# Performance work log

Measured on AMD Instinct MI355X. Metric: run time of the kernel, lower is better.

The kernel has to match this reference:

```python
import jax, jax.numpy as jnp
import numpy as np

P = 16; H_IMG = 384; W_IMG = 384; D = 1024
N_LAYERS = 24; DI = 2048; DS = 16; DTR = 64; DC = 4; EPS = 1e-5


def setup_inputs() -> dict:
    key = jax.random.key(0)
    ks = jax.random.split(key, 12)
    B = 2
    inp = {}
    inp["x"] = jax.random.normal(ks[0], (B, 3, H_IMG, W_IMG), jnp.float32)
    inp["patch_w"] = jax.random.normal(ks[1], (D, 3, P, P), jnp.float32) * 0.02
    inp["patch_b"] = jnp.zeros((D,), jnp.float32)
    inp["pos_embed"] = jax.random.normal(ks[2], (1, (H_IMG // P) * (W_IMG // P), D), jnp.float32) * 0.02
    inp["ln_g"] = jnp.ones((N_LAYERS, D), jnp.float32)
    inp["ln_b"] = jnp.zeros((N_LAYERS, D), jnp.float32)
    inp["in_w"] = jax.random.normal(ks[3], (N_LAYERS, 2 * DI, D), jnp.float32) * 0.02
    inp["conv_w"] = jax.random.normal(ks[4], (N_LAYERS, DI, DC), jnp.float32) * 0.1
    inp["conv_b"] = jnp.zeros((N_LAYERS, DI), jnp.float32)
    inp["xproj_w"] = jax.random.normal(ks[5], (N_LAYERS, DTR + 2 * DS, DI), jnp.float32) * 0.02
    inp["dt_w"] = jax.random.normal(ks[6], (N_LAYERS, DI, DTR), jnp.float32) * 0.02
    inp["dt_b"] = jnp.full((N_LAYERS, DI), -4.0, jnp.float32)  # softplus(-4) ~ 0.018
    inp["A_log"] = jnp.broadcast_to(jnp.log(jnp.arange(1, DS + 1, dtype=jnp.float32)), (N_LAYERS, DI, DS)).copy()
    inp["D_param"] = jnp.ones((N_LAYERS, DI), jnp.float32)
    inp["out_w"] = jax.random.normal(ks[7], (N_LAYERS, D, DI), jnp.float32) * 0.02
    return inp


def _layer_norm(x, g, b):
    mu = jnp.mean(x, axis=-1, keepdims=True)
    var = jnp.var(x, axis=-1, keepdims=True)
    return (x - mu) * jax.lax.rsqrt(var + EPS) * g + b


def _mamba_block(x, p):
    g, bn, Win, Wc, bc, Wxp, Wdt, bdt, Alog, Dd, Wout = p
    u = _layer_norm(x, g, bn)                          # [B,L,D]
    xz = jnp.einsum('bld,ed->ble', u, Win)             # [B,L,2*DI]
    xi, z = jnp.split(xz, 2, axis=-1)
    # causal depthwise conv1d along L (kernel DC=4)
    xt = jnp.moveaxis(xi, 1, 2)                        # [B,DI,L]
    L = xt.shape[-1]
    xpad = jnp.pad(xt, ((0, 0), (0, 0), (DC - 1, 0)))
    xc = sum(Wc[:, k][None, :, None] * xpad[:, :, k:k + L] for k in range(DC)) + bc[None, :, None]
    xc = jax.nn.silu(jnp.moveaxis(xc, 1, 2))           # [B,L,DI]
    dbc = jnp.einsum('bld,ed->ble', xc, Wxp)           # [B,L,DTR+2*DS]
    dt, Bm, Cm = jnp.split(dbc, [DTR, DTR + DS], axis=-1)
    dt = jax.nn.softplus(jnp.einsum('blr,dr->bld', dt, Wdt) + bdt)  # [B,L,DI]
    A = -jnp.exp(Alog)                                 # [DI,DS]
    dA = jnp.exp(dt[..., None] * A)                    # [B,L,DI,DS]
    dBx = (dt * xc)[..., None] * Bm[:, :, None, :]     # [B,L,DI,DS]

    def step(h, inp):
        dA_t, dBx_t, C_t = inp
        h = dA_t * h + dBx_t                           # [B,DI,DS]
        y = jnp.einsum('bds,bs->bd', h, C_t)
        return h, y

    h0 = jnp.zeros((x.shape[0], DI, DS), x.dtype)
    xs = (jnp.moveaxis(dA, 1, 0), jnp.moveaxis(dBx, 1, 0), jnp.moveaxis(Cm, 1, 0))
    _, ys = jax.lax.scan(step, h0, xs)                 # ys: [L,B,DI]
    y = jnp.moveaxis(ys, 0, 1) + Dd * xc
    y = y * jax.nn.silu(z)
    return x + jnp.einsum('ble,de->bld', y, Wout)


def _forward(x, patch_w, patch_b, pos_embed, ln_g, ln_b, in_w, conv_w, conv_b,
             xproj_w, dt_w, dt_b, A_log, D_param, out_w):
    feat = jax.lax.conv_general_dilated(
        x, patch_w, (P, P), 'VALID',
        dimension_numbers=('NCHW', 'OIHW', 'NCHW')) + patch_b[None, :, None, None]
    Bn, Dd, Hh, Ww = feat.shape
    tok = feat.reshape(Bn, Dd, Hh * Ww).transpose(0, 2, 1)  # [B,L,D]
    h0, w0 = H_IMG // P, W_IMG // P
    pe = pos_embed.reshape(1, h0, w0, Dd)
    pe = jax.image.resize(pe, (1, Hh, Ww, Dd), 'bilinear')  # align_corners=False
    tok = tok + pe.reshape(1, Hh * Ww, Dd)
    params = (ln_g, ln_b, in_w, conv_w, conv_b, xproj_w, dt_w, dt_b, A_log, D_param, out_w)

    def layer(carry, p):
        return jax.checkpoint(_mamba_block)(carry, p), None

    tok, _ = jax.lax.scan(layer, tok, params)
    return tok


def reference(x, patch_w, patch_b, pos_embed, ln_g, ln_b, in_w, conv_w, conv_b,
              xproj_w, dt_w, dt_b, A_log, D_param, out_w):
    return _forward(x, patch_w, patch_b, pos_embed, ln_g, ln_b, in_w, conv_w, conv_b,
                    xproj_w, dt_w, dt_b, A_log, D_param, out_w)
```

## Files before the change

### kernel.cpp

```cpp
#include <hip/hip_runtime.h>
#include <hip/hip_bf16.h>
#include <math.h>

#define PATCH   16
#define HIMG    384
#define WIMG    384
#define DMODEL  1024
#define NLAYERS 24
#define DI      2048
#define DSTATE  16
#define DTR     64
#define DC      4
#define LN_EPS  1e-5f
#define BATCH   2
#define GRIDTOK 24
#define LTOK    (GRIDTOK*GRIDTOK)
#define NTOK    (BATCH*LTOK)
#define KPATCH  (3*PATCH*PATCH)
#define NCH     16
#define LC      (LTOK/NCH)
#define PSTRIDE ((size_t)NTOK * 2 * DI)

typedef __attribute__((ext_vector_type(8))) short short8;
typedef __attribute__((ext_vector_type(4))) float f32x4;

__device__ __forceinline__ float sigmoidf_(float v) { return 1.f / (1.f + __expf(-v)); }
__device__ __forceinline__ unsigned short f2bf(float f) {
    __hip_bfloat16 h = __float2bfloat16(f);
    return *(unsigned short*)&h;
}

__device__ __forceinline__ int xcd_swizzle(int orig, int nwg) {
    const int q = nwg >> 3, r = nwg & 7;
    const int xcd = orig & 7, idx = orig >> 3;
    return (xcd < r ? xcd * (q + 1) : r * (q + 1) + (xcd - r) * q) + idx;
}
__device__ __forceinline__ void swz_xyz(int& bx, int& by, int& bz) {
    const int gx = gridDim.x, gy = gridDim.y;
    const int nwg = gx * gy * gridDim.z;
    const int orig = blockIdx.x + gx * (blockIdx.y + gy * blockIdx.z);
    const int id = xcd_swizzle(orig, nwg);
    bx = id % gx;
    const int rest = id / gx;
    by = rest % gy;
    bz = rest / gy;
}

__global__ void f2bf_kernel(const float* __restrict__ in, unsigned short* __restrict__ out, int n4) {
    for (int i = blockIdx.x * blockDim.x + threadIdx.x; i < n4; i += gridDim.x * blockDim.x) {
        const float4 v = ((const float4*)in)[i];
        ushort4 o;
        o.x = f2bf(v.x); o.y = f2bf(v.y); o.z = f2bf(v.z); o.w = f2bf(v.w);
        ((ushort4*)out)[i] = o;
    }
}

__global__ void im2col_kernel(const float* __restrict__ x, unsigned short* __restrict__ xcol) {
    int idx = blockIdx.x * blockDim.x + threadIdx.x;
    if (idx >= NTOK * KPATCH) return;
    int t = idx / KPATCH, k = idx % KPATCH;
    int b = t / LTOK, hw = t % LTOK;
    int h = hw / GRIDTOK, w = hw % GRIDTOK;
    int c = k / (PATCH*PATCH), r = k % (PATCH*PATCH);
    int i = r / PATCH, j = r % PATCH;
    xcol[idx] = f2bf(x[(((size_t)(b*3 + c)*HIMG) + h*PATCH + i)*WIMG + w*PATCH + j]);
}

__global__ __launch_bounds__(256) void layernorm_kernel(
        const float* __restrict__ x, const float* __restrict__ g,
        const float* __restrict__ b, unsigned short* __restrict__ u) {
    const int t = blockIdx.x;
    const int tid = threadIdx.x;
    const float4 xv = ((const float4*)(x + (size_t)t * DMODEL))[tid];
    float s = xv.x + xv.y + xv.z + xv.w;
    float q = xv.x*xv.x + xv.y*xv.y + xv.z*xv.z + xv.w*xv.w;
    #pragma unroll
    for (int off = 32; off >= 1; off >>= 1) {
        s += __shfl_xor(s, off);
        q += __shfl_xor(q, off);
    }
    __shared__ float red[8];
    if ((tid & 63) == 0) { red[tid >> 6] = s; red[4 + (tid >> 6)] = q; }
    __syncthreads();
    s = red[0] + red[1] + red[2] + red[3];
    q = red[4] + red[5] + red[6] + red[7];
    const float mu   = s * (1.f / DMODEL);
    const float var  = q * (1.f / DMODEL) - mu * mu;
    const float rstd = rsqrtf(var + LN_EPS);
    const float4 gv = ((const float4*)g)[tid];
    const float4 bv = ((const float4*)b)[tid];
    ushort4 o;
    o.x = f2bf((xv.x - mu) * rstd * gv.x + bv.x);
    o.y = f2bf((xv.y - mu) * rstd * gv.y + bv.y);
    o.z = f2bf((xv.z - mu) * rstd * gv.z + bv.z);
    o.w = f2bf((xv.w - mu) * rstd * gv.w + bv.w);
    ((ushort4*)(u + (size_t)t * DMODEL))[tid] = o;
}

__global__ __launch_bounds__(256) void gemm_mfma_bt(
        const unsigned short* __restrict__ A, int lda,
        const float* __restrict__ B, int ldb,
        float* __restrict__ C, int M, int N, int Ksub) {
    __shared__ unsigned short As[128 * 64];
    __shared__ unsigned short Bs[128 * 64];
    int bx, by, bz;
    swz_xyz(bx, by, bz);
    const int tid = threadIdx.x;
    const int m0 = bx * 128;
    const int n0 = by * 128;
    const int koff = bz * Ksub;
    C += (size_t)bz * M * N;

    const int lane = tid & 63;
    const int wid  = tid >> 6;
    const int wm = (wid >> 1) * 64;
    const int wn = (wid & 1) * 64;
    const int fr = lane & 15;
    const int cb = lane >> 4;

    const int srow = tid >> 3;
    const int skc  = tid & 7;

    f32x4 acc[4][4];
    #pragma unroll
    for (int i = 0; i < 4; ++i)
        #pragma unroll
        for (int j = 0; j < 4; ++j) acc[i][j] = (f32x4){0.f, 0.f, 0.f, 0.f};

    uint4  areg[4];
    float4 breg[4][2];

    const int nk = Ksub / 64;
    #pragma unroll
    for (int i = 0; i < 4; ++i) {
        const int r = srow + 32 * i;
        areg[i] = *(const uint4*)(A + (size_t)(m0 + r) * lda + koff + skc * 8);
        const float* bp = B + (size_t)(n0 + r) * ldb + koff + skc * 8;
        breg[i][0] = *(const float4*)bp;
        breg[i][1] = *(const float4*)(bp + 4);
    }

    for (int ks = 0; ks < nk; ++ks) {
        __syncthreads();
        #pragma unroll
        for (int i = 0; i < 4; ++i) {
            const int r = srow + 32 * i;
            const int idx = r * 64 + ((skc ^ (r & 7)) << 3);
            *(uint4*)&As[idx] = areg[i];
            const float* bf = (const float*)&breg[i][0];
            short8 hv;
            #pragma unroll
            for (int j = 0; j < 8; ++j) hv[j] = (short)f2bf(bf[j]);
            *(short8*)&Bs[idx] = hv;
        }
        __syncthreads();
        if (ks + 1 < nk) {
            const int k1 = koff + (ks + 1) * 64;
            #pragma unroll
            for (int i = 0; i < 4; ++i) {
                const int r = srow + 32 * i;
                areg[i] = *(const uint4*)(A + (size_t)(m0 + r) * lda + k1 + skc * 8);
                const float* bp = B + (size_t)(n0 + r) * ldb + k1 + skc * 8;
                breg[i][0] = *(const float4*)bp;
                breg[i][1] = *(const float4*)(bp + 4);
            }
        }
        #pragma unroll
        for (int kk = 0; kk < 2; ++kk) {
            short8 af[4], bfr[4];
            #pragma unroll
            for (int mi = 0; mi < 4; ++mi) {
                const int row = wm + mi * 16 + fr;
                af[mi] = *(const short8*)&As[row * 64 + (((kk * 4 + cb) ^ (row & 7)) << 3)];
            }
            #pragma unroll
            for (int ni = 0; ni < 4; ++ni) {
                const int row = wn + ni * 16 + fr;
                bfr[ni] = *(const short8*)&Bs[row * 64 + (((kk * 4 + cb) ^ (row & 7)) << 3)];
            }
            #pragma unroll
            for (int mi = 0; mi < 4; ++mi)
                #pragma unroll
                for (int ni = 0; ni < 4; ++ni)
                    acc[mi][ni] = __builtin_amdgcn_mfma_f32_16x16x32_bf16(
                        af[mi], bfr[ni], acc[mi][ni], 0, 0, 0);
        }
    }

    #pragma unroll
    for (int mi = 0; mi < 4; ++mi) {
        const int rbase = m0 + wm + mi * 16 + cb * 4;
        #pragma unroll
        for (int ni = 0; ni < 4; ++ni) {
            const int col = n0 + wn + ni * 16 + fr;
            #pragma unroll
            for (int j = 0; j < 4; ++j)
                C[(size_t)(rbase + j) * N + col] = acc[mi][ni][j];
        }
    }
}

template<int EPI>
__global__ __launch_bounds__(256) void gemm_bb(
        const unsigned short* __restrict__ A, int lda,
        const unsigned short* __restrict__ B, int ldb,
        float* __restrict__ C, int M, int N, int Ksub,
        const float* __restrict__ bias, const float* __restrict__ aux) {
    __shared__ unsigned short As[128 * 64];
    __shared__ unsigned short Bs[128 * 64];
    int bx, by, bz;
    swz_xyz(bx, by, bz);
    const int tid = threadIdx.x;
    const int m0 = bx * 128;
    const int n0 = by * 128;

    const int lane = tid & 63;
    const int wid  = tid >> 6;
    const int wm = (wid >> 1) * 64;
    const int wn = (wid & 1) * 64;
    const int fr = lane & 15;
    const int cb = lane >> 4;
    const int srow = tid >> 3;
    const int skc  = tid & 7;

    f32x4 acc[4][4];
    #pragma unroll
    for (int i = 0; i < 4; ++i)
        #pragma unroll
        for (int j = 0; j < 4; ++j) acc[i][j] = (f32x4){0.f, 0.f, 0.f, 0.f};

    uint4 areg[4], breg[4];
    const int nk = Ksub / 64;
    #pragma unroll
    for (int i = 0; i < 4; ++i) {
        const int r = srow + 32 * i;
        areg[i] = *(const uint4*)(A + (size_t)(m0 + r) * lda + skc * 8);
        breg[i] = *(const uint4*)(B + (size_t)(n0 + r) * ldb + skc * 8);
    }

    for (int ks = 0; ks < nk; ++ks) {
        __syncthreads();
        #pragma unroll
        for (int i = 0; i < 4; ++i) {
            const int r = srow + 32 * i;
            const int idx = r * 64 + ((skc ^ (r & 7)) << 3);
            *(uint4*)&As[idx] = areg[i];
            *(uint4*)&Bs[idx] = breg[i];
        }
        __syncthreads();
        if (ks + 1 < nk) {
            const int k1 = (ks + 1) * 64;
            #pragma unroll
            for (int i = 0; i < 4; ++i) {
                const int r = srow + 32 * i;
                areg[i] = *(const uint4*)(A + (size_t)(m0 + r) * lda + k1 + skc * 8);
                breg[i] = *(const uint4*)(B + (size_t)(n0 + r) * ldb + k1 + skc * 8);
            }
        }
        #pragma unroll
        for (int kk = 0; kk < 2; ++kk) {
            short8 af[4], bfr[4];
            #pragma unroll
            for (int mi = 0; mi < 4; ++mi) {
                const int row = wm + mi * 16 + fr;
                af[mi] = *(const short8*)&As[row * 64 + (((kk * 4 + cb) ^ (row & 7)) << 3)];
            }
            #pragma unroll
            for (int ni = 0; ni < 4; ++ni) {
                const int row = wn + ni * 16 + fr;
                bfr[ni] = *(const short8*)&Bs[row * 64 + (((kk * 4 + cb) ^ (row & 7)) << 3)];
            }
            #pragma unroll
            for (int mi = 0; mi < 4; ++mi)
                #pragma unroll
                for (int ni = 0; ni < 4; ++ni)
                    acc[mi][ni] = __builtin_amdgcn_mfma_f32_16x16x32_bf16(
                        af[mi], bfr[ni], acc[mi][ni], 0, 0, 0);
        }
    }

    #pragma unroll
    for (int mi = 0; mi < 4; ++mi) {
        const int rbase = m0 + wm + mi * 16 + cb * 4;
        #pragma unroll
        for (int ni = 0; ni < 4; ++ni) {
            const int col = n0 + wn + ni * 16 + fr;
            #pragma unroll
            for (int j = 0; j < 4; ++j) {
                float v = acc[mi][ni][j];
                if (EPI == 1) {
                    v += bias[col];
                    v = (v > 20.f) ? v : log1pf(__expf(v));
                } else if (EPI == 2) {
                    v += bias[col] + aux[(size_t)((rbase + j) % LTOK) * DMODEL + col];
                }
                C[(size_t)(rbase + j) * N + col] = v;
            }
        }
    }
}

__global__ __launch_bounds__(256) void gemm_xproj(
        const unsigned short* __restrict__ A,
        const unsigned short* __restrict__ B,
        float* __restrict__ C) {
    __shared__ unsigned short As[128 * 64];
    __shared__ unsigned short Bs[96 * 64];
    int bx, by, bz;
    swz_xyz(bx, by, bz);
    const int tid = threadIdx.x;
    const int m0 = bx * 128;
    const int koff = by * (DI / 8);
    C += (size_t)by * NTOK * 96;

    const int lane = tid & 63;
    const int wid  = tid >> 6;
    const int wm = wid * 32;
    const int fr = lane & 15;
    const int cb = lane >> 4;
    const int srow = tid >> 3;
    const int skc  = tid & 7;

    f32x4 acc[2][6];
    #pragma unroll
    for (int i = 0; i < 2; ++i)
        #pragma unroll
        for (int j = 0; j < 6; ++j) acc[i][j] = (f32x4){0.f, 0.f, 0.f, 0.f};

    uint4 areg[4], breg[3];
    #pragma unroll
    for (int i = 0; i < 4; ++i)
        areg[i] = *(const uint4*)(A + (size_t)(m0 + srow + 32 * i) * DI + koff + skc * 8);
    #pragma unroll
    for (int i = 0; i < 3; ++i) {
        const int idx = tid + 256 * i;
        breg[i] = *(const uint4*)(B + (size_t)(idx >> 3) * DI + koff + (idx & 7) * 8);
    }

    const int nk = (DI / 8) / 64;
    for (int ks = 0; ks < nk; ++ks) {
        __syncthreads();
        #pragma unroll
        for (int i = 0; i < 4; ++i) {
            const int r = srow + 32 * i;
            *(uint4*)&As[r * 64 + ((skc ^ (r & 7)) << 3)] = areg[i];
        }
        #pragma unroll
        for (int i = 0; i < 3; ++i) {
            const int idx = tid + 256 * i;
            const int r = idx >> 3, kc = idx & 7;
            *(uint4*)&Bs[r * 64 + ((kc ^ (r & 7)) << 3)] = breg[i];
        }
        __syncthreads();
        if (ks + 1 < nk) {
            const int k1 = koff + (ks + 1) * 64;
            #pragma unroll
            for (int i = 0; i < 4; ++i)
                areg[i] = *(const uint4*)(A + (size_t)(m0 + srow + 32 * i) * DI + k1 + skc * 8);
            #pragma unroll
            for (int i = 0; i < 3; ++i) {
                const int idx = tid + 256 * i;
                breg[i] = *(const uint4*)(B + (size_t)(idx >> 3) * DI + k1 + (idx & 7) * 8);
            }
        }
        #pragma unroll
        for (int kk = 0; kk < 2; ++kk) {
            short8 af[2], bfr[6];
            #pragma unroll
            for (int mi = 0; mi < 2; ++mi) {
                const int row = wm + mi * 16 + fr;
                af[mi] = *(const short8*)&As[row * 64 + (((kk * 4 + cb) ^ (row & 7)) << 3)];
            }
            #pragma unroll
            for (int ni = 0; ni < 6; ++ni) {
                const int row = ni * 16 + fr;
                bfr[ni] = *(const short8*)&Bs[row * 64 + (((kk * 4 + cb) ^ (row & 7)) << 3)];
            }
            #pragma unroll
            for (int mi = 0; mi < 2; ++mi)
                #pragma unroll
                for (int ni = 0; ni < 6; ++ni)
                    acc[mi][ni] = __builtin_amdgcn_mfma_f32_16x16x32_bf16(
                        af[mi], bfr[ni], acc[mi][ni], 0, 0, 0);
        }
    }

    #pragma unroll
    for (int mi = 0; mi < 2; ++mi) {
        const int rbase = m0 + wm + mi * 16 + cb * 4;
        #pragma unroll
        for (int ni = 0; ni < 6; ++ni) {
            const int col = ni * 16 + fr;
            #pragma unroll
            for (int j = 0; j < 4; ++j)
                C[(size_t)(rbase + j) * 96 + col] = acc[mi][ni][j];
        }
    }
}

__global__ void reduce8_kernel(const float* __restrict__ part, float* __restrict__ out,
                               unsigned short* __restrict__ out64, int n) {
    int i = blockIdx.x * blockDim.x + threadIdx.x;
    if (i >= n) return;
    float s = 0.f;
    #pragma unroll
    for (int z = 0; z < 8; ++z) s += part[(size_t)z * n + i];
    out[i] = s;
    const int col = i % 96;
    if (col < 64) out64[(i / 96) * 64 + col] = f2bf(s);
}

__global__ void conv1d_silu_kernel(const float* __restrict__ xzP,
                                   const float* __restrict__ wc,
                                   const float* __restrict__ bc,
                                   float* __restrict__ xc,
                                   unsigned short* __restrict__ xc_bf) {
    int idx = blockIdx.x * blockDim.x + threadIdx.x;
    if (idx >= NTOK * DI) return;
    const int t = idx >> 11;
    const int e = idx & (DI - 1);
    const int l = t % LTOK;
    const float4 w = *(const float4*)(wc + e * DC);
    const float* xp0 = xzP + (size_t)t * (2*DI) + e;
    const float* xp1 = xp0 + PSTRIDE;
    float acc = bc[e] + w.w * (xp0[0] + xp1[0]);
    if (l >= 1) acc += w.z * (xp0[-(2*DI)]   + xp1[-(2*DI)]);
    if (l >= 2) acc += w.y * (xp0[-2*(2*DI)] + xp1[-2*(2*DI)]);
    if (l >= 3) acc += w.x * (xp0[-3*(2*DI)] + xp1[-3*(2*DI)]);
    const float r = acc * sigmoidf_(acc);
    xc[idx] = r;
    xc_bf[idx] = f2bf(r);
}

__global__ __launch_bounds__(256) void scan_pass1(
        const float* __restrict__ dt, const float* __restrict__ xc,
        const float* __restrict__ dbc, const float* __restrict__ Alog,
        float* __restrict__ Fst, float* __restrict__ sdt) {
    const int tid = threadIdx.x;
    const int e  = blockIdx.x * 256 + tid;
    const int c  = blockIdx.y;
    const int b  = blockIdx.z;
    const int l0 = c * LC;
    const size_t tb = (size_t)b * LTOK + l0;

    __shared__ float Bs[LC][16];
    for (int idx = tid; idx < LC * 16; idx += 256) {
        const int row = idx >> 4, s = idx & 15;
        Bs[row][s] = dbc[(tb + row) * 96 + 64 + s];
    }

    float Aval[DSTATE];
    {
        const float* ap = Alog + (size_t)e * DSTATE;
        #pragma unroll
        for (int s = 0; s < DSTATE; ++s) Aval[s] = -__expf(ap[s]);
    }
    __syncthreads();

    const float* dtp = dt + tb * DI + e;
    const float* xcp = xc + tb * DI + e;
    float h[DSTATE];
    #pragma unroll
    for (int s = 0; s < DSTATE; ++s) h[s] = 0.f;
    float sum_dt = 0.f;

    float dtv = dtp[0], xcv = xcp[0];
    for (int l = 0; l < LC; ++l) {
        float dtn = 0.f, xcn = 0.f;
        if (l + 1 < LC) { dtn = dtp[(size_t)(l+1) * DI]; xcn = xcp[(size_t)(l+1) * DI]; }
        sum_dt += dtv;
        const float dx = dtv * xcv;
        const float4* brow = (const float4*)&Bs[l][0];
        const float4 b0 = brow[0], b1 = brow[1], b2 = brow[2], b3 = brow[3];
        const float bb[16] = {b0.x,b0.y,b0.z,b0.w, b1.x,b1.y,b1.z,b1.w,
                              b2.x,b2.y,b2.z,b2.w, b3.x,b3.y,b3.z,b3.w};
        #pragma unroll
        for (int s = 0; s < DSTATE; ++s)
            h[s] = fmaf(__expf(dtv * Aval[s]), h[s], dx * bb[s]);
        dtv = dtn; xcv = xcn;
    }

    float4* Fp = (float4*)(Fst + ((((size_t)b * NCH + c) * DI) + e) * DSTATE);
    #pragma unroll
    for (int q = 0; q < 4; ++q)
        Fp[q] = make_float4(h[q*4+0], h[q*4+1], h[q*4+2], h[q*4+3]);
    sdt[((size_t)b * NCH + c) * DI + e] = sum_dt;
}

__global__ __launch_bounds__(256) void scan_pass3(
        const float* __restrict__ dt, const float* __restrict__ xc,
        const float* __restrict__ dbc, const float* __restrict__ xzP,
        const float* __restrict__ Alog, const float* __restrict__ Dp,
        const float* __restrict__ Fst, const float* __restrict__ sdt,
        unsigned short* __restrict__ y) {
    const int tid = threadIdx.x;
    const int e  = blockIdx.x * 256 + tid;
    const int c  = blockIdx.y;
    const int b  = blockIdx.z;
    const int l0 = c * LC;
    const size_t tb = (size_t)b * LTOK + l0;

    __shared__ float BCs[LC][32];
    for (int idx = tid; idx < LC * 32; idx += 256) {
        const int row = idx >> 5, col = idx & 31;
        BCs[row][col] = dbc[(tb + row) * 96 + 64 + col];
    }

    float Aval[DSTATE];
    {
        const float* ap = Alog + (size_t)e * DSTATE;
        #pragma unroll
        for (int s = 0; s < DSTATE; ++s) Aval[s] = -__expf(ap[s]);
    }
    const float Dv = Dp[e];

    float h[DSTATE];
    #pragma unroll
    for (int s = 0; s < DSTATE; ++s) h[s] = 0.f;
    for (int c2 = 0; c2 < c; ++c2) {
        const size_t base = ((size_t)b * NCH + c2) * DI + e;
        const float sd = sdt[base];
        const float4* Fp = (const float4*)(Fst + base * DSTATE);
        const float4 f0 = Fp[0], f1 = Fp[1], f2 = Fp[2], f3 = Fp[3];
        const float ff[16] = {f0.x,f0.y,f0.z,f0.w, f1.x,f1.y,f1.z,f1.w,
                              f2.x,f2.y,f2.z,f2.w, f3.x,f3.y,f3.z,f3.w};
        #pragma unroll
        for (int s = 0; s < DSTATE; ++s)
            h[s] = fmaf(__expf(Aval[s] * sd), h[s], ff[s]);
    }
    __syncthreads();

    const float* dtp = dt + tb * DI + e;
    const float* xcp = xc + tb * DI + e;
    const float* zp0 = xzP + tb * (2*DI) + DI + e;
    const float* zp1 = zp0 + PSTRIDE;
    unsigned short* yp = y + tb * DI + e;

    float dtv = dtp[0], xcv = xcp[0], zv = zp0[0] + zp1[0];
    for (int l = 0; l < LC; ++l) {
        float dtn = 0.f, xcn = 0.f, zn = 0.f;
        if (l + 1 < LC) {
            dtn = dtp[(size_t)(l+1) * DI];
            xcn = xcp[(size_t)(l+1) * DI];
            zn  = zp0[(size_t)(l+1) * (2*DI)] + zp1[(size_t)(l+1) * (2*DI)];
        }
        const float dx = dtv * xcv;
        const float4* brow = (const float4*)&BCs[l][0];
        const float4 b0 = brow[0], b1 = brow[1], b2 = brow[2], b3 = brow[3];
        const float4 c0 = brow[4], c1 = brow[5], c2 = brow[6], c3 = brow[7];
        const float bb[16] = {b0.x,b0.y,b0.z,b0.w, b1.x,b1.y,b1.z,b1.w,
                              b2.x,b2.y,b2.z,b2.w, b3.x,b3.y,b3.z,b3.w};
        const float cc[16] = {c0.x,c0.y,c0.z,c0.w, c1.x,c1.y,c1.z,c1.w,
                              c2.x,c2.y,c2.z,c2.w, c3.x,c3.y,c3.z,c3.w};
        float yv = 0.f;
        #pragma unroll
        for (int s = 0; s < DSTATE; ++s) {
            h[s] = fmaf(__expf(dtv * Aval[s]), h[s], dx * bb[s]);
            yv = fmaf(h[s], cc[s], yv);
        }
        yp[(size_t)l * DI] = f2bf((yv + Dv * xcv) * (zv * sigmoidf_(zv)));
        dtv = dtn; xcv = xcn; zv = zn;
    }
}

template<bool DO_LN>
__global__ __launch_bounds__(256) void reduce8_ln_kernel(
        const float* __restrict__ part, float* __restrict__ tok,
        const float* __restrict__ g, const float* __restrict__ b,
        unsigned short* __restrict__ u) {
    const int t = blockIdx.x;
    const int tid = threadIdx.x;
    const int n4 = NTOK * DMODEL / 4;
    const int i = t * 256 + tid;
    float4 tv = ((float4*)tok)[i];
    #pragma unroll
    for (int z = 0; z < 8; ++z) {
        const float4 p = ((const float4*)part)[(size_t)z * n4 + i];
        tv.x += p.x; tv.y += p.y; tv.z += p.z; tv.w += p.w;
    }
    ((float4*)tok)[i] = tv;
    if (DO_LN) {
        float s = tv.x + tv.y + tv.z + tv.w;
        float q = tv.x*tv.x + tv.y*tv.y + tv.z*tv.z + tv.w*tv.w;
        #pragma unroll
        for (int off = 32; off >= 1; off >>= 1) {
            s += __shfl_xor(s, off);
            q += __shfl_xor(q, off);
        }
        __shared__ float red[8];
        if ((tid & 63) == 0) { red[tid >> 6] = s; red[4 + (tid >> 6)] = q; }
        __syncthreads();
        s = red[0] + red[1] + red[2] + red[3];
        q = red[4] + red[5] + red[6] + red[7];
        const float mu   = s * (1.f / DMODEL);
        const float var  = q * (1.f / DMODEL) - mu * mu;
        const float rstd = rsqrtf(var + LN_EPS);
        const float4 gv = ((const float4*)g)[tid];
        const float4 bv = ((const float4*)b)[tid];
        ushort4 o;
        o.x = f2bf((tv.x - mu) * rstd * gv.x + bv.x);
        o.y = f2bf((tv.y - mu) * rstd * gv.y + bv.y);
        o.z = f2bf((tv.z - mu) * rstd * gv.z + bv.z);
        o.w = f2bf((tv.w - mu) * rstd * gv.w + bv.w);
        ((ushort4*)(u + (size_t)t * DMODEL))[tid] = o;
    }
}

extern "C" void kernel_launch(void* const* d_in, const int* in_sizes, int n_in,
                              void* d_out, int out_size, void* d_ws, size_t ws_size,
                              hipStream_t stream) {
    const float* x       = (const float*)d_in[0];
    const float* patch_w = (const float*)d_in[1];
    const float* patch_b = (const float*)d_in[2];
    const float* pos     = (const float*)d_in[3];
    const float* ln_g    = (const float*)d_in[4];
    const float* ln_b    = (const float*)d_in[5];
    const float* in_w    = (const float*)d_in[6];
    const float* conv_w  = (const float*)d_in[7];
    const float* conv_b  = (const float*)d_in[8];
    const float* xproj_w = (const float*)d_in[9];
    const float* dt_w    = (const float*)d_in[10];
    const float* dt_b    = (const float*)d_in[11];
    const float* A_log   = (const float*)d_in[12];
    const float* D_par   = (const float*)d_in[13];
    const float* out_w   = (const float*)d_in[14];

    float* tok = (float*)d_out;
    float* ws  = (float*)d_ws;
    float* xzP  = ws;  ws += 2 * PSTRIDE;
    float* xc   = ws;  ws += (size_t)NTOK * DI;
    float* dbcP = ws;  ws += (size_t)8 * NTOK * 96;
    float* dbc  = ws;  ws += (size_t)NTOK * 96;
    float* dtb  = ws;  ws += (size_t)NTOK * DI;
    float* Fst  = ws;  ws += (size_t)BATCH * NCH * DI * DSTATE;
    float* sdt  = ws;  ws += (size_t)BATCH * NCH * DI;
    unsigned short* us = (unsigned short*)ws;
    unsigned short* Xcol_bf  = us; us += (size_t)NTOK * KPATCH;
    unsigned short* u_bf     = us; us += (size_t)NTOK * DMODEL;
    unsigned short* xc_bf    = us; us += (size_t)NTOK * DI;
    unsigned short* yb_bf    = us; us += (size_t)NTOK * DI;
    unsigned short* dbc64_bf = us; us += (size_t)NTOK * 64;
    unsigned short* wxpb  = us; us += (size_t)NLAYERS * 96 * DI;
    unsigned short* wdtb  = us; us += (size_t)NLAYERS * DI * DTR;
    unsigned short* wpb   = us; us += (size_t)DMODEL * KPATCH;

    f2bf_kernel<<<1024, 256, 0, stream>>>(xproj_w, wxpb, NLAYERS*96*DI/4);
    f2bf_kernel<<<1024, 256, 0, stream>>>(dt_w,    wdtb, NLAYERS*DI*DTR/4);
    f2bf_kernel<<<256,  256, 0, stream>>>(patch_w, wpb,  DMODEL*KPATCH/4);

    im2col_kernel<<<(NTOK*KPATCH + 255)/256, 256, 0, stream>>>(x, Xcol_bf);
    gemm_bb<2><<<dim3(NTOK/128, DMODEL/128), 256, 0, stream>>>(
        Xcol_bf, KPATCH, wpb, KPATCH, tok, NTOK, DMODEL, KPATCH, patch_b, pos);

    layernorm_kernel<<<NTOK, 256, 0, stream>>>(tok, ln_g, ln_b, u_bf);

    for (int layer = 0; layer < NLAYERS; ++layer) {
        const float* Win = in_w  + (size_t)layer * 2 * DI * DMODEL;
        const float* Wo  = out_w + (size_t)layer * DMODEL * DI;
        const unsigned short* Wxp = wxpb + (size_t)layer * 96 * DI;
        const unsigned short* Wdt = wdtb + (size_t)layer * DI * DTR;
        const float* Wc  = conv_w + (size_t)layer * DI * DC;
        const float* Bc  = conv_b + (size_t)layer * DI;
        const float* Bdt = dt_b   + (size_t)layer * DI;
        const float* Al  = A_log  + (size_t)layer * DI * DSTATE;
        const float* Dd  = D_par  + (size_t)layer * DI;

        gemm_mfma_bt<<<dim3(NTOK/128, (2*DI)/128, 2), 256, 0, stream>>>(
            u_bf, DMODEL, Win, DMODEL, xzP, NTOK, 2*DI, DMODEL/2);
        conv1d_silu_kernel<<<(NTOK*DI + 255)/256, 256, 0, stream>>>(xzP, Wc, Bc, xc, xc_bf);
        gemm_xproj<<<dim3(NTOK/128, 8), 256, 0, stream>>>(xc_bf, Wxp, dbcP);
        reduce8_kernel<<<(NTOK*96 + 255)/256, 256, 0, stream>>>(dbcP, dbc, dbc64_bf, NTOK*96);
        gemm_bb<1><<<dim3(NTOK/128, DI/128), 256, 0, stream>>>(
            dbc64_bf, 64, Wdt, DTR, dtb, NTOK, DI, DTR, Bdt, nullptr);
        scan_pass1<<<dim3(DI/256, NCH, BATCH), 256, 0, stream>>>(
            dtb, xc, dbc, Al, Fst, sdt);
        scan_pass3<<<dim3(DI/256, NCH, BATCH), 256, 0, stream>>>(
            dtb, xc, dbc, xzP, Al, Dd, Fst, sdt, yb_bf);
        gemm_mfma_bt<<<dim3(NTOK/128, DMODEL/128, 8), 256, 0, stream>>>(
            yb_bf, DI, Wo, DI, xzP, NTOK, DMODEL, DI/8);
        if (layer < NLAYERS - 1)
            reduce8_ln_kernel<true><<<NTOK, 256, 0, stream>>>(
                xzP, tok, ln_g + (size_t)(layer+1) * DMODEL, ln_b + (size_t)(layer+1) * DMODEL, u_bf);
        else
            reduce8_ln_kernel<false><<<NTOK, 256, 0, stream>>>(
                xzP, tok, nullptr, nullptr, u_bf);
    }
}
```

Measured before the change: 4.495 ms.

## Retile fp32-weight GEMM to 128x64x128 tiles and cut split-K partials

Changes the bf16×fp32 GEMM tile from 128x128 with K-step 64 to 128x64 with K-step 128, with a new B-loading layout. The in-projection drops split-K entirely, which removes the summing of two partial buffers in the conv and scan kernels. The out-projection goes from 8-way to 4-way split-K, so the reduce+layernorm kernel reads half as many partials. The goal is less partial-sum traffic and fewer reduction reads. The cost is longer K loops per block and more A reloads, since each A tile is now shared across fewer N columns.

```diff
diff --git a/kernel.cpp b/kernel.cpp
--- a/kernel.cpp
+++ b/kernel.cpp
@@ -19,7 +19,6 @@
 #define KPATCH  (3*PATCH*PATCH)
 #define NCH     16
 #define LC      (LTOK/NCH)
-#define PSTRIDE ((size_t)NTOK * 2 * DI)
 
 typedef __attribute__((ext_vector_type(8))) short short8;
 typedef __attribute__((ext_vector_type(4))) float f32x4;
@@ -101,87 +100,99 @@
         const unsigned short* __restrict__ A, int lda,
         const float* __restrict__ B, int ldb,
         float* __restrict__ C, int M, int N, int Ksub) {
-    __shared__ unsigned short As[128 * 64];
-    __shared__ unsigned short Bs[128 * 64];
+    __shared__ unsigned short As[128 * 128];
+    __shared__ unsigned short Bs[64 * 128];
     int bx, by, bz;
     swz_xyz(bx, by, bz);
     const int tid = threadIdx.x;
     const int m0 = bx * 128;
-    const int n0 = by * 128;
+    const int n0 = by * 64;
     const int koff = bz * Ksub;
     C += (size_t)bz * M * N;
 
     const int lane = tid & 63;
     const int wid  = tid >> 6;
     const int wm = (wid >> 1) * 64;
-    const int wn = (wid & 1) * 64;
+    const int wn = (wid & 1) * 32;
     const int fr = lane & 15;
     const int cb = lane >> 4;
 
-    const int srow = tid >> 3;
-    const int skc  = tid & 7;
-
-    f32x4 acc[4][4];
+    const int srowA = tid >> 3;
+    const int skcA  = tid & 7;
+    const int browB = tid >> 2;
+    const int sb0   = (tid & 3) * 4;
+
+    f32x4 acc[4][2];
     #pragma unroll
     for (int i = 0; i < 4; ++i)
         #pragma unroll
-        for (int j = 0; j < 4; ++j) acc[i][j] = (f32x4){0.f, 0.f, 0.f, 0.f};
-
-    uint4  areg[4];
-    float4 breg[4][2];
-
-    const int nk = Ksub / 64;
+        for (int j = 0; j < 2; ++j) acc[i][j] = (f32x4){0.f, 0.f, 0.f, 0.f};
+
+    uint4  areg[4][2];
+    float4 bregf[8];
+
+    const int nk = Ksub / 128;
     #pragma unroll
     for (int i = 0; i < 4; ++i) {
-        const int r = srow + 32 * i;
-        areg[i] = *(const uint4*)(A + (size_t)(m0 + r) * lda + koff + skc * 8);
-        const float* bp = B + (size_t)(n0 + r) * ldb + koff + skc * 8;
-        breg[i][0] = *(const float4*)bp;
-        breg[i][1] = *(const float4*)(bp + 4);
+        const int r = srowA + 32 * i;
+        const unsigned short* ap = A + (size_t)(m0 + r) * lda + koff;
+        areg[i][0] = *(const uint4*)(ap + skcA * 8);
+        areg[i][1] = *(const uint4*)(ap + (skcA + 8) * 8);
+    }
+    {
+        const float* bp = B + (size_t)(n0 + browB) * ldb + koff + (tid & 3) * 32;
+        #pragma unroll
+        for (int j = 0; j < 8; ++j) bregf[j] = *(const float4*)(bp + j * 4);
     }
 
     for (int ks = 0; ks < nk; ++ks) {
         __syncthreads();
         #pragma unroll
         for (int i = 0; i < 4; ++i) {
-            const int r = srow + 32 * i;
-            const int idx = r * 64 + ((skc ^ (r & 7)) << 3);
-            *(uint4*)&As[idx] = areg[i];
-            const float* bf = (const float*)&breg[i][0];
+            const int r = srowA + 32 * i;
+            *(uint4*)&As[r * 128 + ((skcA       ^ (r & 7)) << 3)] = areg[i][0];
+            *(uint4*)&As[r * 128 + (((skcA + 8) ^ (r & 7)) << 3)] = areg[i][1];
+        }
+        #pragma unroll
+        for (int q = 0; q < 4; ++q) {
+            const float* f = (const float*)&bregf[2 * q];
             short8 hv;
             #pragma unroll
-            for (int j = 0; j < 8; ++j) hv[j] = (short)f2bf(bf[j]);
-            *(short8*)&Bs[idx] = hv;
+            for (int j = 0; j < 8; ++j) hv[j] = (short)f2bf(f[j]);
+            const int slot = sb0 + q;
+            *(short8*)&Bs[browB * 128 + ((slot ^ (browB & 7)) << 3)] = hv;
         }
         __syncthreads();
         if (ks + 1 < nk) {
-            const int k1 = koff + (ks + 1) * 64;
+            const int k1 = koff + (ks + 1) * 128;
             #pragma unroll
             for (int i = 0; i < 4; ++i) {
-                const int r = srow + 32 * i;
-                areg[i] = *(const uint4*)(A + (size_t)(m0 + r) * lda + k1 + skc * 8);
-                const float* bp = B + (size_t)(n0 + r) * ldb + k1 + skc * 8;
-                breg[i][0] = *(const float4*)bp;
-                breg[i][1] = *(const float4*)(bp + 4);
-            }
-        }
-        #pragma unroll
-        for (int kk = 0; kk < 2; ++kk) {
-            short8 af[4], bfr[4];
+                const int r = srowA + 32 * i;
+                const unsigned short* ap = A + (size_t)(m0 + r) * lda + k1;
+                areg[i][0] = *(const uint4*)(ap + skcA * 8);
+                areg[i][1] = *(const uint4*)(ap + (skcA + 8) * 8);
+            }
+            const float* bp = B + (size_t)(n0 + browB) * ldb + k1 + (tid & 3) * 32;
+            #pragma unroll
+            for (int j = 0; j < 8; ++j) bregf[j] = *(const float4*)(bp + j * 4);
+        }
+        #pragma unroll
+        for (int kk = 0; kk < 4; ++kk) {
+            short8 af[4], bfr[2];
             #pragma unroll
             for (int mi = 0; mi < 4; ++mi) {
                 const int row = wm + mi * 16 + fr;
-                af[mi] = *(const short8*)&As[row * 64 + (((kk * 4 + cb) ^ (row & 7)) << 3)];
-            }
-            #pragma unroll
-            for (int ni = 0; ni < 4; ++ni) {
+                af[mi] = *(const short8*)&As[row * 128 + (((kk * 4 + cb) ^ (row & 7)) << 3)];
+            }
+            #pragma unroll
+            for (int ni = 0; ni < 2; ++ni) {
                 const int row = wn + ni * 16 + fr;
-                bfr[ni] = *(const short8*)&Bs[row * 64 + (((kk * 4 + cb) ^ (row & 7)) << 3)];
+                bfr[ni] = *(const short8*)&Bs[row * 128 + (((kk * 4 + cb) ^ (row & 7)) << 3)];
             }
             #pragma unroll
             for (int mi = 0; mi < 4; ++mi)
                 #pragma unroll
-                for (int ni = 0; ni < 4; ++ni)
+                for (int ni = 0; ni < 2; ++ni)
                     acc[mi][ni] = __builtin_amdgcn_mfma_f32_16x16x32_bf16(
                         af[mi], bfr[ni], acc[mi][ni], 0, 0, 0);
         }
@@ -191,7 +202,7 @@
     for (int mi = 0; mi < 4; ++mi) {
         const int rbase = m0 + wm + mi * 16 + cb * 4;
         #pragma unroll
-        for (int ni = 0; ni < 4; ++ni) {
+        for (int ni = 0; ni < 2; ++ni) {
             const int col = n0 + wn + ni * 16 + fr;
             #pragma unroll
             for (int j = 0; j < 4; ++j)
@@ -410,7 +421,7 @@
     if (col < 64) out64[(i / 96) * 64 + col] = f2bf(s);
 }
 
-__global__ void conv1d_silu_kernel(const float* __restrict__ xzP,
+__global__ void conv1d_silu_kernel(const float* __restrict__ xz,
                                    const float* __restrict__ wc,
                                    const float* __restrict__ bc,
                                    float* __restrict__ xc,
@@ -421,12 +432,11 @@
     const int e = idx & (DI - 1);
     const int l = t % LTOK;
     const float4 w = *(const float4*)(wc + e * DC);
-    const float* xp0 = xzP + (size_t)t * (2*DI) + e;
-    const float* xp1 = xp0 + PSTRIDE;
-    float acc = bc[e] + w.w * (xp0[0] + xp1[0]);
-    if (l >= 1) acc += w.z * (xp0[-(2*DI)]   + xp1[-(2*DI)]);
-    if (l >= 2) acc += w.y * (xp0[-2*(2*DI)] + xp1[-2*(2*DI)]);
-    if (l >= 3) acc += w.x * (xp0[-3*(2*DI)] + xp1[-3*(2*DI)]);
+    const float* xp = xz + (size_t)t * (2*DI) + e;
+    float acc = bc[e] + w.w * xp[0];
+    if (l >= 1) acc += w.z * xp[-(2*DI)];
+    if (l >= 2) acc += w.y * xp[-2*(2*DI)];
+    if (l >= 3) acc += w.x * xp[-3*(2*DI)];
     const float r = acc * sigmoidf_(acc);
     xc[idx] = r;
     xc_bf[idx] = f2bf(r);
@@ -489,7 +499,7 @@
 
 __global__ __launch_bounds__(256) void scan_pass3(
         const float* __restrict__ dt, const float* __restrict__ xc,
-        const float* __restrict__ dbc, const float* __restrict__ xzP,
+        const float* __restrict__ dbc, const float* __restrict__ xz,
         const float* __restrict__ Alog, const float* __restrict__ Dp,
         const float* __restrict__ Fst, const float* __restrict__ sdt,
         unsigned short* __restrict__ y) {
@@ -532,17 +542,16 @@
 
     const float* dtp = dt + tb * DI + e;
     const float* xcp = xc + tb * DI + e;
-    const float* zp0 = xzP + tb * (2*DI) + DI + e;
-    const float* zp1 = zp0 + PSTRIDE;
+    const float* zp  = xz + tb * (2*DI) + DI + e;
     unsigned short* yp = y + tb * DI + e;
 
-    float dtv = dtp[0], xcv = xcp[0], zv = zp0[0] + zp1[0];
+    float dtv = dtp[0], xcv = xcp[0], zv = zp[0];
     for (int l = 0; l < LC; ++l) {
         float dtn = 0.f, xcn = 0.f, zn = 0.f;
         if (l + 1 < LC) {
             dtn = dtp[(size_t)(l+1) * DI];
             xcn = xcp[(size_t)(l+1) * DI];
-            zn  = zp0[(size_t)(l+1) * (2*DI)] + zp1[(size_t)(l+1) * (2*DI)];
+            zn  = zp[(size_t)(l+1) * (2*DI)];
         }
         const float dx = dtv * xcv;
         const float4* brow = (const float4*)&BCs[l][0];
@@ -564,7 +573,7 @@
 }
 
 template<bool DO_LN>
-__global__ __launch_bounds__(256) void reduce8_ln_kernel(
+__global__ __launch_bounds__(256) void reduce4_ln_kernel(
         const float* __restrict__ part, float* __restrict__ tok,
         const float* __restrict__ g, const float* __restrict__ b,
         unsigned short* __restrict__ u) {
@@ -574,7 +583,7 @@
     const int i = t * 256 + tid;
     float4 tv = ((float4*)tok)[i];
     #pragma unroll
-    for (int z = 0; z < 8; ++z) {
+    for (int z = 0; z < 4; ++z) {
         const float4 p = ((const float4*)part)[(size_t)z * n4 + i];
         tv.x += p.x; tv.y += p.y; tv.z += p.z; tv.w += p.w;
     }
@@ -627,7 +636,7 @@
 
     float* tok = (float*)d_out;
     float* ws  = (float*)d_ws;
-    float* xzP  = ws;  ws += 2 * PSTRIDE;
+    float* xz   = ws;  ws += (size_t)NTOK * 2 * DI;
     float* xc   = ws;  ws += (size_t)NTOK * DI;
     float* dbcP = ws;  ws += (size_t)8 * NTOK * 96;
     float* dbc  = ws;  ws += (size_t)NTOK * 96;
@@ -665,9 +674,9 @@
         const float* Al  = A_log  + (size_t)layer * DI * DSTATE;
         const float* Dd  = D_par  + (size_t)layer * DI;
 
-        gemm_mfma_bt<<<dim3(NTOK/128, (2*DI)/128, 2), 256, 0, stream>>>(
-            u_bf, DMODEL, Win, DMODEL, xzP, NTOK, 2*DI, DMODEL/2);
-        conv1d_silu_kernel<<<(NTOK*DI + 255)/256, 256, 0, stream>>>(xzP, Wc, Bc, xc, xc_bf);
+        gemm_mfma_bt<<<dim3(NTOK/128, (2*DI)/64, 1), 256, 0, stream>>>(
+            u_bf, DMODEL, Win, DMODEL, xz, NTOK, 2*DI, DMODEL);
+        conv1d_silu_kernel<<<(NTOK*DI + 255)/256, 256, 0, stream>>>(xz, Wc, Bc, xc, xc_bf);
         gemm_xproj<<<dim3(NTOK/128, 8), 256, 0, stream>>>(xc_bf, Wxp, dbcP);
         reduce8_kernel<<<(NTOK*96 + 255)/256, 256, 0, stream>>>(dbcP, dbc, dbc64_bf, NTOK*96);
         gemm_bb<1><<<dim3(NTOK/128, DI/128), 256, 0, stream>>>(
@@ -675,14 +684,14 @@
         scan_pass1<<<dim3(DI/256, NCH, BATCH), 256, 0, stream>>>(
             dtb, xc, dbc, Al, Fst, sdt);
         scan_pass3<<<dim3(DI/256, NCH, BATCH), 256, 0, stream>>>(
-            dtb, xc, dbc, xzP, Al, Dd, Fst, sdt, yb_bf);
-        gemm_mfma_bt<<<dim3(NTOK/128, DMODEL/128, 8), 256, 0, stream>>>(
-            yb_bf, DI, Wo, DI, xzP, NTOK, DMODEL, DI/8);
+            dtb, xc, dbc, xz, Al, Dd, Fst, sdt, yb_bf);
+        gemm_mfma_bt<<<dim3(NTOK/128, DMODEL/64, 4), 256, 0, stream>>>(
+            yb_bf, DI, Wo, DI, xz, NTOK, DMODEL, DI/4);
         if (layer < NLAYERS - 1)
-            reduce8_ln_kernel<true><<<NTOK, 256, 0, stream>>>(
-                xzP, tok, ln_g + (size_t)(layer+1) * DMODEL, ln_b + (size_t)(layer+1) * DMODEL, u_bf);
+            reduce4_ln_kernel<true><<<NTOK, 256, 0, stream>>>(
+                xz, tok, ln_g + (size_t)(layer+1) * DMODEL, ln_b + (size_t)(layer+1) * DMODEL, u_bf);
         else
-            reduce8_ln_kernel<false><<<NTOK, 256, 0, stream>>>(
-                xzP, tok, nullptr, nullptr, u_bf);
-    }
-}
+            reduce4_ln_kernel<false><<<NTOK, 256, 0, stream>>>(
+                xz, tok, nullptr, nullptr, u_bf);
+    }
+}
```

After: 5.807 ms. 29.2% more time.

## Retile x_proj split-K GEMM and add dedicated dt projection kernel

Applied to the files above, without the earlier changes.

The x_proj GEMM now uses 64-row tiles and a split-K factor of 16 instead of 128-row tiles with split 8. That launches four times as many workgroups, each doing a shorter K loop, and the reduction kernel now sums 16 partials. The dt projection (K=64) moves from the generic gemm_bb path to a specialized single-stage kernel with 128x64 tiles, which doubles its grid and drops the K loop. The intent is better CU occupancy for these small GEMMs, at the cost of more partial-sum traffic and a larger workspace.

```diff
diff --git a/kernel.cpp b/kernel.cpp
--- a/kernel.cpp
+++ b/kernel.cpp
@@ -20,6 +20,7 @@
 #define NCH     16
 #define LC      (LTOK/NCH)
 #define PSTRIDE ((size_t)NTOK * 2 * DI)
+#define XP_SK   16
 
 typedef __attribute__((ext_vector_type(8))) short short8;
 typedef __attribute__((ext_vector_type(4))) float f32x4;
@@ -288,62 +289,55 @@
             #pragma unroll
             for (int j = 0; j < 4; ++j) {
                 float v = acc[mi][ni][j];
-                if (EPI == 1) {
-                    v += bias[col];
-                    v = (v > 20.f) ? v : log1pf(__expf(v));
-                } else if (EPI == 2) {
+                if (EPI == 2)
                     v += bias[col] + aux[(size_t)((rbase + j) % LTOK) * DMODEL + col];
-                }
                 C[(size_t)(rbase + j) * N + col] = v;
             }
         }
     }
 }
 
-__global__ __launch_bounds__(256) void gemm_xproj(
+__global__ __launch_bounds__(256) void gemm_xproj64(
         const unsigned short* __restrict__ A,
         const unsigned short* __restrict__ B,
         float* __restrict__ C) {
-    __shared__ unsigned short As[128 * 64];
+    __shared__ unsigned short As[64 * 64];
     __shared__ unsigned short Bs[96 * 64];
     int bx, by, bz;
     swz_xyz(bx, by, bz);
     const int tid = threadIdx.x;
-    const int m0 = bx * 128;
-    const int koff = by * (DI / 8);
+    const int m0 = bx * 64;
+    const int koff = by * (DI / XP_SK);
     C += (size_t)by * NTOK * 96;
 
     const int lane = tid & 63;
     const int wid  = tid >> 6;
-    const int wm = wid * 32;
+    const int wm = wid * 16;
     const int fr = lane & 15;
     const int cb = lane >> 4;
     const int srow = tid >> 3;
     const int skc  = tid & 7;
 
-    f32x4 acc[2][6];
-    #pragma unroll
-    for (int i = 0; i < 2; ++i)
-        #pragma unroll
-        for (int j = 0; j < 6; ++j) acc[i][j] = (f32x4){0.f, 0.f, 0.f, 0.f};
-
-    uint4 areg[4], breg[3];
-    #pragma unroll
-    for (int i = 0; i < 4; ++i)
-        areg[i] = *(const uint4*)(A + (size_t)(m0 + srow + 32 * i) * DI + koff + skc * 8);
+    f32x4 acc[6];
+    #pragma unroll
+    for (int j = 0; j < 6; ++j) acc[j] = (f32x4){0.f, 0.f, 0.f, 0.f};
+
+    uint4 areg[2], breg[3];
+    areg[0] = *(const uint4*)(A + (size_t)(m0 + srow) * DI + koff + skc * 8);
+    areg[1] = *(const uint4*)(A + (size_t)(m0 + srow + 32) * DI + koff + skc * 8);
     #pragma unroll
     for (int i = 0; i < 3; ++i) {
         const int idx = tid + 256 * i;
         breg[i] = *(const uint4*)(B + (size_t)(idx >> 3) * DI + koff + (idx & 7) * 8);
     }
 
-    const int nk = (DI / 8) / 64;
+    const int nk = (DI / XP_SK) / 64;
     for (int ks = 0; ks < nk; ++ks) {
         __syncthreads();
-        #pragma unroll
-        for (int i = 0; i < 4; ++i) {
-            const int r = srow + 32 * i;
-            *(uint4*)&As[r * 64 + ((skc ^ (r & 7)) << 3)] = areg[i];
+        {
+            const int r0 = srow, r1 = srow + 32;
+            *(uint4*)&As[r0 * 64 + ((skc ^ (r0 & 7)) << 3)] = areg[0];
+            *(uint4*)&As[r1 * 64 + ((skc ^ (r1 & 7)) << 3)] = areg[1];
         }
         #pragma unroll
         for (int i = 0; i < 3; ++i) {
@@ -354,9 +348,8 @@
         __syncthreads();
         if (ks + 1 < nk) {
             const int k1 = koff + (ks + 1) * 64;
-            #pragma unroll
-            for (int i = 0; i < 4; ++i)
-                areg[i] = *(const uint4*)(A + (size_t)(m0 + srow + 32 * i) * DI + k1 + skc * 8);
+            areg[0] = *(const uint4*)(A + (size_t)(m0 + srow) * DI + k1 + skc * 8);
+            areg[1] = *(const uint4*)(A + (size_t)(m0 + srow + 32) * DI + k1 + skc * 8);
             #pragma unroll
             for (int i = 0; i < 3; ++i) {
                 const int idx = tid + 256 * i;
@@ -365,46 +358,115 @@
         }
         #pragma unroll
         for (int kk = 0; kk < 2; ++kk) {
-            short8 af[2], bfr[6];
-            #pragma unroll
-            for (int mi = 0; mi < 2; ++mi) {
-                const int row = wm + mi * 16 + fr;
-                af[mi] = *(const short8*)&As[row * 64 + (((kk * 4 + cb) ^ (row & 7)) << 3)];
-            }
+            const int arow = wm + fr;
+            const short8 af = *(const short8*)&As[arow * 64 + (((kk * 4 + cb) ^ (arow & 7)) << 3)];
+            short8 bfr[6];
             #pragma unroll
             for (int ni = 0; ni < 6; ++ni) {
                 const int row = ni * 16 + fr;
                 bfr[ni] = *(const short8*)&Bs[row * 64 + (((kk * 4 + cb) ^ (row & 7)) << 3)];
             }
             #pragma unroll
-            for (int mi = 0; mi < 2; ++mi)
-                #pragma unroll
-                for (int ni = 0; ni < 6; ++ni)
-                    acc[mi][ni] = __builtin_amdgcn_mfma_f32_16x16x32_bf16(
-                        af[mi], bfr[ni], acc[mi][ni], 0, 0, 0);
-        }
-    }
-
-    #pragma unroll
-    for (int mi = 0; mi < 2; ++mi) {
+            for (int ni = 0; ni < 6; ++ni)
+                acc[ni] = __builtin_amdgcn_mfma_f32_16x16x32_bf16(af, bfr[ni], acc[ni], 0, 0, 0);
+        }
+    }
+
+    const int rbase = m0 + wm + cb * 4;
+    #pragma unroll
+    for (int ni = 0; ni < 6; ++ni) {
+        const int col = ni * 16 + fr;
+        #pragma unroll
+        for (int j = 0; j < 4; ++j)
+            C[(size_t)(rbase + j) * 96 + col] = acc[ni][j];
+    }
+}
+
+__global__ __launch_bounds__(256) void gemm_dt(
+        const unsigned short* __restrict__ A,
+        const unsigned short* __restrict__ B,
+        float* __restrict__ C, const float* __restrict__ bias) {
+    __shared__ unsigned short As[128 * 64];
+    __shared__ unsigned short Bs[64 * 64];
+    int bx, by, bz;
+    swz_xyz(bx, by, bz);
+    const int tid = threadIdx.x;
+    const int m0 = bx * 128;
+    const int n0 = by * 64;
+
+    const int lane = tid & 63;
+    const int wid  = tid >> 6;
+    const int wm = (wid >> 1) * 64;
+    const int wn = (wid & 1) * 32;
+    const int fr = lane & 15;
+    const int cb = lane >> 4;
+    const int srow = tid >> 3;
+    const int skc  = tid & 7;
+
+    #pragma unroll
+    for (int i = 0; i < 4; ++i) {
+        const int r = srow + 32 * i;
+        const uint4 v = *(const uint4*)(A + (size_t)(m0 + r) * 64 + skc * 8);
+        *(uint4*)&As[r * 64 + ((skc ^ (r & 7)) << 3)] = v;
+    }
+    #pragma unroll
+    for (int i = 0; i < 2; ++i) {
+        const int r = srow + 32 * i;
+        const uint4 v = *(const uint4*)(B + (size_t)(n0 + r) * 64 + skc * 8);
+        *(uint4*)&Bs[r * 64 + ((skc ^ (r & 7)) << 3)] = v;
+    }
+    __syncthreads();
+
+    f32x4 acc[4][2];
+    #pragma unroll
+    for (int i = 0; i < 4; ++i)
+        #pragma unroll
+        for (int j = 0; j < 2; ++j) acc[i][j] = (f32x4){0.f, 0.f, 0.f, 0.f};
+
+    #pragma unroll
+    for (int kk = 0; kk < 2; ++kk) {
+        short8 af[4], bfr[2];
+        #pragma unroll
+        for (int mi = 0; mi < 4; ++mi) {
+            const int row = wm + mi * 16 + fr;
+            af[mi] = *(const short8*)&As[row * 64 + (((kk * 4 + cb) ^ (row & 7)) << 3)];
+        }
+        #pragma unroll
+        for (int ni = 0; ni < 2; ++ni) {
+            const int row = wn + ni * 16 + fr;
+            bfr[ni] = *(const short8*)&Bs[row * 64 + (((kk * 4 + cb) ^ (row & 7)) << 3)];
+        }
+        #pragma unroll
+        for (int mi = 0; mi < 4; ++mi)
+            #pragma unroll
+            for (int ni = 0; ni < 2; ++ni)
+                acc[mi][ni] = __builtin_amdgcn_mfma_f32_16x16x32_bf16(
+                    af[mi], bfr[ni], acc[mi][ni], 0, 0, 0);
+    }
+
+    #pragma unroll
+    for (int mi = 0; mi < 4; ++mi) {
         const int rbase = m0 + wm + mi * 16 + cb * 4;
         #pragma unroll
-        for (int ni = 0; ni < 6; ++ni) {
-            const int col = ni * 16 + fr;
-            #pragma unroll
-            for (int j = 0; j < 4; ++j)
-                C[(size_t)(rbase + j) * 96 + col] = acc[mi][ni][j];
-        }
-    }
-}
-
-__global__ void reduce8_kernel(const float* __restrict__ part, float* __restrict__ out,
-                               unsigned short* __restrict__ out64, int n) {
+        for (int ni = 0; ni < 2; ++ni) {
+            const int col = n0 + wn + ni * 16 + fr;
+            #pragma unroll
+            for (int j = 0; j < 4; ++j) {
+                float v = acc[mi][ni][j] + bias[col];
+                v = (v > 20.f) ? v : log1pf(__expf(v));
+                C[(size_t)(rbase + j) * DI + col] = v;
+            }
+        }
+    }
+}
+
+__global__ void reduce16_kernel(const float* __restrict__ part, float* __restrict__ out,
+                                unsigned short* __restrict__ out64, int n) {
     int i = blockIdx.x * blockDim.x + threadIdx.x;
     if (i >= n) return;
     float s = 0.f;
     #pragma unroll
-    for (int z = 0; z < 8; ++z) s += part[(size_t)z * n + i];
+    for (int z = 0; z < XP_SK; ++z) s += part[(size_t)z * n + i];
     out[i] = s;
     const int col = i % 96;
     if (col < 64) out64[(i / 96) * 64 + col] = f2bf(s);
@@ -629,7 +691,7 @@
     float* ws  = (float*)d_ws;
     float* xzP  = ws;  ws += 2 * PSTRIDE;
     float* xc   = ws;  ws += (size_t)NTOK * DI;
-    float* dbcP = ws;  ws += (size_t)8 * NTOK * 96;
+    float* dbcP = ws;  ws += (size_t)XP_SK * NTOK * 96;
     float* dbc  = ws;  ws += (size_t)NTOK * 96;
     float* dtb  = ws;  ws += (size_t)NTOK * DI;
     float* Fst  = ws;  ws += (size_t)BATCH * NCH * DI * DSTATE;
@@ -668,10 +730,9 @@
         gemm_mfma_bt<<<dim3(NTOK/128, (2*DI)/128, 2), 256, 0, stream>>>(
             u_bf, DMODEL, Win, DMODEL, xzP, NTOK, 2*DI, DMODEL/2);
         conv1d_silu_kernel<<<(NTOK*DI + 255)/256, 256, 0, stream>>>(xzP, Wc, Bc, xc, xc_bf);
-        gemm_xproj<<<dim3(NTOK/128, 8), 256, 0, stream>>>(xc_bf, Wxp, dbcP);
-        reduce8_kernel<<<(NTOK*96 + 255)/256, 256, 0, stream>>>(dbcP, dbc, dbc64_bf, NTOK*96);
-        gemm_bb<1><<<dim3(NTOK/128, DI/128), 256, 0, stream>>>(
-            dbc64_bf, 64, Wdt, DTR, dtb, NTOK, DI, DTR, Bdt, nullptr);
+        gemm_xproj64<<<dim3(NTOK/64, XP_SK), 256, 0, stream>>>(xc_bf, Wxp, dbcP);
+        reduce16_kernel<<<(NTOK*96 + 255)/256, 256, 0, stream>>>(dbcP, dbc, dbc64_bf, NTOK*96);
+        gemm_dt<<<dim3(NTOK/128, DI/64), 256, 0, stream>>>(dbc64_bf, Wdt, dtb, Bdt);
         scan_pass1<<<dim3(DI/256, NCH, BATCH), 256, 0, stream>>>(
             dtb, xc, dbc, Al, Fst, sdt);
         scan_pass3<<<dim3(DI/256, NCH, BATCH), 256, 0, stream>>>(
```

Result: faster. 3.961 ms (-11.9%).
